# Optimization experiments

Hardware: AMD Instinct MI355X
Metric: run time of the kernel (lower is better)

## Reference

```python
import jax, jax.numpy as jnp
import numpy as np

N, D, H, C = 4096, 4096, 256, 16
NNZ_ATTR, E, NNZ_JM, NNZ_JA = 262144, 131072, 400000, 80000


def setup_inputs() -> dict:
    key = jax.random.key(0)
    ks = jax.random.split(key, 8)
    return {
        "attr_row": jax.random.randint(ks[0], (NNZ_ATTR,), 0, N),
        "attr_col": jax.random.randint(ks[1], (NNZ_ATTR,), 0, D),
        "edge_idx": jax.random.randint(ks[2], (2, E), 0, N),
        "j_mask_idx": jax.random.randint(ks[3], (2, NNZ_JM), 0, N),
        "jaug_mask_idx": jax.random.randint(ks[4], (2, NNZ_JA), 0, N),
        "lin1_w": jax.random.normal(ks[5], (H, D), dtype=jnp.float32) * (1.0 / np.sqrt(D)),
        "lin2_w": jax.random.normal(ks[6], (C, H), dtype=jnp.float32) * (1.0 / np.sqrt(H)),
        "bias2": jax.random.normal(ks[7], (C,), dtype=jnp.float32) * 0.01,
        "n": N,
        "d": D,
    }


def _gcn_norm_dense(a, n):
    # add remaining self loops (binary adjacency -> set diagonal to 1)
    idx = jnp.arange(n)
    a = a.at[idx, idx].set(1.0)
    # PyG gcn_norm: deg = scatter_add(weight, col) = column sums
    deg = a.sum(axis=0)
    dinv = jnp.where(deg > 0, jax.lax.rsqrt(deg), 0.0)
    # out[i] = sum_j dinv[i]*dinv[j]*A[j,i]*x[j]  ->  An = Dinv @ A^T @ Dinv
    return (dinv[:, None] * a.T) * dinv[None, :]


def reference(attr_row, attr_col, edge_idx, j_mask_idx, jaug_mask_idx,
              lin1_w, lin2_w, bias2, n, d):
    # --- edge augmentation: (edges AND J_mask) OR JAug_mask ---
    a = jnp.zeros((n, n), jnp.float32).at[edge_idx[0], edge_idx[1]].set(1.0)
    jm = jnp.zeros((n, n), bool).at[j_mask_idx[0], j_mask_idx[1]].set(True)
    ja = jnp.zeros((n, n), bool).at[jaug_mask_idx[0], jaug_mask_idx[1]].set(True)
    a_aug = jnp.maximum(jnp.where(jm, a, 0.0), ja.astype(jnp.float32))

    # --- layer 1: spmm(sparse binary X, W1^T), gcn_norm, propagate (no bias) ---
    x = jnp.zeros((n, d), jnp.float32).at[attr_row, attr_col].add(1.0)
    h = x @ lin1_w.T                     # [n, H]
    an = _gcn_norm_dense(a_aug, n)       # [n, n] normalized adjacency
    h = jax.nn.relu(an @ h)              # propagate + relu
    # dropout is identity in eval mode

    # --- layer 2: standard GCNConv with bias ---
    h2 = h @ lin2_w.T                    # [n, C]
    out = an @ h2 + bias2
    return out
```

## Files before the change

kernel.cpp:

```cpp
#include <hip/hip_runtime.h>

#define N_      4096
#define D_      4096
#define H_      256
#define C_      16
#define NNZ_ATTR 262144
#define E_      131072
#define NNZ_JM  400000
#define NNZ_JA  80000
#define WORDS   128
#define ADJ_STRIDE 128
#define ASTR    128
#define NT      256

typedef _Float16 half8v __attribute__((ext_vector_type(8)));
typedef _Float16 half2v __attribute__((ext_vector_type(2)));

#define OFF_EBT  ((size_t)0)
#define OFF_ABT  ((size_t)(2u<<20))
#define OFF_CNT  ((size_t)(4u<<20))
#define OFF_DINV (OFF_CNT + (size_t)(256u<<10))
#define OFF_DEG  (OFF_DINV + (size_t)(16u<<10))
#define OFF_CCOL (OFF_DEG + (size_t)(16u<<10))
#define OFF_ADJ  (OFF_CCOL + (size_t)(2u<<20))
#define OFF_W1T  (OFF_ADJ + (size_t)(2u<<20))
#define OFF_H1   (OFF_W1T + (size_t)(2u<<20))
#define OFF_H2   (OFF_H1  + (size_t)(2u<<20))

#define ZERO_BYTES ((size_t)((4u<<20)+(256u<<10)))
#define ZB_BLOCKS  1088
#define TR_BLOCKS  1024

#define SB_EDGE  1024
#define SB_JA    1536
#define SB_DIAG  1849
#define SB_TOTAL 1865

__global__ void k_pre(const float* __restrict__ w1, _Float16* __restrict__ w1t,
                      uint4* __restrict__ zp) {
    __shared__ float tile[32][33];
    int b = blockIdx.x, t = threadIdx.x;
    if (b < ZB_BLOCKS) {
        zp[(size_t)b * NT + t] = make_uint4(0u, 0u, 0u, 0u);
    } else {
        int bb = b - ZB_BLOCKS;
        int gx = bb & 127, gy = bb >> 7;
        int tx = t & 31, ty = t >> 5;
        int col = gx * 32 + tx;
        #pragma unroll
        for (int j = 0; j < 4; ++j)
            tile[ty + j * 8][tx] = w1[(size_t)(gy * 32 + ty + j * 8) * D_ + col];
        __syncthreads();
        int ocol = gy * 32 + tx;
        #pragma unroll
        for (int j = 0; j < 4; ++j)
            w1t[(size_t)(gx * 32 + ty + j * 8) * H_ + ocol] = (_Float16)tile[tx][ty + j * 8];
    }
}

__global__ void k_scat1(const int* __restrict__ attr_row, const int* __restrict__ attr_col,
                        const int* __restrict__ edge, const int* __restrict__ jaug,
                        unsigned* __restrict__ ebt, unsigned* __restrict__ abt,
                        unsigned* __restrict__ cnt, unsigned* __restrict__ ccol) {
    const int b = blockIdx.x, t = threadIdx.x;
    if (b < SB_EDGE) {
        int i = b * NT + t;
        int r = attr_row[i];
        unsigned pos = atomicAdd(&cnt[r << 4], 1u);
        if (pos < ASTR) ccol[(size_t)r * ASTR + pos] = (unsigned)attr_col[i];
    } else if (b < SB_JA) {
        int j = (b - SB_EDGE) * NT + t;
        int p = edge[j], q = edge[E_ + j];
        atomicOr(&ebt[(size_t)q * WORDS + (p >> 5)], 1u << (p & 31));
    } else if (b < SB_DIAG) {
        int j = (b - SB_JA) * NT + t;
        if (j < NNZ_JA) {
            int p = jaug[j], q = jaug[NNZ_JA + j];
            atomicOr(&abt[(size_t)q * WORDS + (p >> 5)], 1u << (p & 31));
        }
    } else {
        int r = (b - SB_DIAG) * NT + t;
        atomicOr(&abt[(size_t)r * WORDS + (r >> 5)], 1u << (r & 31));
    }
}

__global__ void k_scat2(const int* __restrict__ jmsk,
                        const unsigned* __restrict__ ebt, unsigned* __restrict__ abt) {
    int i = blockIdx.x * NT + threadIdx.x;
    if (i >= NNZ_JM) return;
    int p = jmsk[i], q = jmsk[NNZ_JM + i];
    size_t w = (size_t)q * WORDS + (p >> 5);
    if ((ebt[w] >> (p & 31)) & 1u)
        atomicOr(&abt[w], 1u << (p & 31));
}

__global__ void k_rowh1(const unsigned* __restrict__ abt, const unsigned* __restrict__ cnt,
                        const unsigned* __restrict__ ccol, const _Float16* __restrict__ w1t,
                        float* __restrict__ dinv, int* __restrict__ deg,
                        int* __restrict__ adj, _Float16* __restrict__ h1s) {
    __shared__ unsigned cols[128];
    __shared__ float part[4][2][32][8];
    __shared__ float sdinv[4];
    const int b = blockIdx.x, t = threadIdx.x;
    int wv = t >> 6, lane = t & 63;
    int q = 4 * b + wv;
    {
        uint2 m2 = ((const uint2*)(abt + (size_t)q * WORDS))[lane];
        unsigned w0 = m2.x, w1b = m2.y;
        int c = __popc(w0) + __popc(w1b);
        int pre = c;
        #pragma unroll
        for (int d2 = 1; d2 < 64; d2 <<= 1) {
            int x = __shfl_up(pre, d2);
            if (lane >= d2) pre += x;
        }
        int excl = pre - c;
        int total = __shfl(pre, 63);
        if (lane == 0) {
            float dv = rsqrtf((float)total);
            dinv[q] = dv;
            sdinv[wv] = dv;
            deg[q] = total < ADJ_STRIDE ? total : ADJ_STRIDE;
        }
        unsigned idx = (unsigned)excl;
        int* arow = adj + (size_t)q * ADJ_STRIDE;
        int base0 = lane * 64;
        while (w0)  { int bp = __ffs(w0) - 1;  w0  &= w0 - 1;  if (idx < ADJ_STRIDE) arow[idx] = base0 + bp;      ++idx; }
        while (w1b) { int bp = __ffs(w1b) - 1; w1b &= w1b - 1; if (idx < ADJ_STRIDE) arow[idx] = base0 + 32 + bp; ++idx; }
    }
    __syncthreads();
    int g = t >> 6, hw = (t >> 5) & 1, l32 = t & 31;
    for (int i = 0; i < 4; ++i) {
        int r = 4 * b + i;
        int m = (int)min(cnt[r << 4], (unsigned)ASTR);
        if (t < m) cols[t] = ccol[(size_t)r * ASTR + t];
        __syncthreads();
        float acc[8];
        #pragma unroll
        for (int e = 0; e < 8; ++e) acc[e] = 0.f;
        int sub = (g << 1) + hw;
        for (int j = 0; j < m; j += 8) {
            int jc = j + sub;
            if (jc < m) {
                unsigned c = cols[jc];
                half8v v = *(const half8v*)(w1t + (size_t)c * H_ + l32 * 8);
                #pragma unroll
                for (int e = 0; e < 8; ++e) acc[e] += (float)v[e];
            }
        }
        #pragma unroll
        for (int e = 0; e < 8; ++e) part[g][hw][l32][e] = acc[e];
        __syncthreads();
        int l = t >> 3, e = t & 7;
        float s = 0.f;
        #pragma unroll
        for (int gg = 0; gg < 4; ++gg) {
            s += part[gg][0][l][e];
            s += part[gg][1][l][e];
        }
        h1s[(size_t)r * H_ + t] = (_Float16)(s * sdinv[i]);
        __syncthreads();
    }
}

__global__ void k_prop1(const int* __restrict__ adj, const int* __restrict__ deg,
                        const float* __restrict__ dinv, const _Float16* __restrict__ h1s,
                        const float* __restrict__ w2, float* __restrict__ h2s) {
    __shared__ int adj_s[128];
    __shared__ float partial2[2][256];
    __shared__ float hrow[256];
    __shared__ float partial[16][17];
    const int b = blockIdx.x, t = threadIdx.x;
    int g2 = t >> 7, tt = t & 127;
    int c = t & 15, gg = t >> 4;
    float w2r[16];
    #pragma unroll
    for (int kk = 0; kk < 16; ++kk) w2r[kk] = w2[(size_t)c * H_ + gg * 16 + kk];
    for (int i = 0; i < 4; ++i) {
        int q = 4 * b + i;
        __syncthreads();
        if (t < ADJ_STRIDE) adj_s[t] = adj[(size_t)q * ADJ_STRIDE + t];
        __syncthreads();
        int dg = deg[q];
        float ax = 0.f, ay = 0.f;
        int j = g2;
        for (; j + 2 < dg; j += 4) {
            int p0 = adj_s[j], p1 = adj_s[j + 2];
            half2v v0 = *(const half2v*)(h1s + (size_t)p0 * H_ + tt * 2);
            half2v v1 = *(const half2v*)(h1s + (size_t)p1 * H_ + tt * 2);
            ax += (float)v0[0] + (float)v1[0];
            ay += (float)v0[1] + (float)v1[1];
        }
        for (; j < dg; j += 2) {
            int p0 = adj_s[j];
            half2v v0 = *(const half2v*)(h1s + (size_t)p0 * H_ + tt * 2);
            ax += (float)v0[0];
            ay += (float)v0[1];
        }
        partial2[g2][2 * tt]     = ax;
        partial2[g2][2 * tt + 1] = ay;
        __syncthreads();
        float dq = dinv[q];
        hrow[t] = fmaxf((partial2[0][t] + partial2[1][t]) * dq, 0.f);
        __syncthreads();
        float p = 0.f;
        #pragma unroll
        for (int kk = 0; kk < 16; ++kk) p += hrow[gg * 16 + kk] * w2r[kk];
        partial[gg][c] = p;
        __syncthreads();
        if (t < 16) {
            float s = 0.f;
            #pragma unroll
            for (int g3 = 0; g3 < 16; ++g3) s += partial[g3][t];
            h2s[(size_t)q * C_ + t] = s * dq;
        }
    }
}

__global__ void k_prop2(const int* __restrict__ adj, const int* __restrict__ deg,
                        const float* __restrict__ dinv, const float* __restrict__ h2s,
                        const float* __restrict__ bias, float* __restrict__ out) {
    const int b = blockIdx.x, t = threadIdx.x;
    int wv = t >> 6, lane = t & 63;
    int q = 4 * b + wv;
    int c = lane & 15, prt = lane >> 4;
    int dg = deg[q];
    const int* arow = adj + (size_t)q * ADJ_STRIDE;
    float acc = 0.f;
    for (int j = prt; j < dg; j += 4)
        acc += h2s[(size_t)arow[j] * C_ + c];
    acc += __shfl_down(acc, 32);
    acc += __shfl_down(acc, 16);
    if (lane < 16)
        out[(size_t)q * C_ + c] = dinv[q] * acc + bias[c];
}


extern "C" void kernel_launch(void* const* d_in, const int* in_sizes, int n_in,
                              void* d_out, int out_size, void* d_ws, size_t ws_size,
                              hipStream_t stream) {
    const int*   attr_row = (const int*)d_in[0];
    const int*   attr_col = (const int*)d_in[1];
    const int*   edge     = (const int*)d_in[2];
    const int*   jmsk     = (const int*)d_in[3];
    const int*   jaug     = (const int*)d_in[4];
    const float* w1       = (const float*)d_in[5];
    const float* w2       = (const float*)d_in[6];
    const float* bias2    = (const float*)d_in[7];
    float*       out      = (float*)d_out;

    char* ws = (char*)d_ws;
    unsigned*  ebt  = (unsigned*)(ws + OFF_EBT);
    unsigned*  abt  = (unsigned*)(ws + OFF_ABT);
    unsigned*  cnt  = (unsigned*)(ws + OFF_CNT);
    float*     dinv = (float*)(ws + OFF_DINV);
    int*       deg  = (int*)(ws + OFF_DEG);
    unsigned*  ccol = (unsigned*)(ws + OFF_CCOL);
    int*       adj  = (int*)(ws + OFF_ADJ);
    _Float16*  w1t  = (_Float16*)(ws + OFF_W1T);
    _Float16*  h1s  = (_Float16*)(ws + OFF_H1);
    float*     h2s  = (float*)(ws + OFF_H2);

    k_pre<<<ZB_BLOCKS + TR_BLOCKS, NT, 0, stream>>>(w1, w1t, (uint4*)d_ws);
    k_scat1<<<SB_TOTAL, NT, 0, stream>>>(attr_row, attr_col, edge, jaug,
                                         ebt, abt, cnt, ccol);
    k_scat2<<<(NNZ_JM + NT - 1) / NT, NT, 0, stream>>>(jmsk, ebt, abt);
    k_rowh1<<<N_ / 4, NT, 0, stream>>>(abt, cnt, ccol, w1t, dinv, deg, adj, h1s);
    k_prop1<<<N_ / 4, NT, 0, stream>>>(adj, deg, dinv, h1s, w2, h2s);
    k_prop2<<<N_ / 4, NT, 0, stream>>>(adj, deg, dinv, h2s, bias2, out);
}
```

Before: 75.46 us.

## Replace atomic bitmask scatters with dense byte maps and slot-claim dedup

After: 80.56 us. 6.8% more time.

```diff
diff --git a/kernel.cpp b/kernel.cpp
--- a/kernel.cpp
+++ b/kernel.cpp
@@ -10,40 +10,47 @@
 #define NNZ_JA  80000
 #define WORDS   128
 #define ADJ_STRIDE 128
-#define ASTR    128
 #define NT      256
+#define MAXCOLS 208
 
 typedef _Float16 half8v __attribute__((ext_vector_type(8)));
 typedef _Float16 half2v __attribute__((ext_vector_type(2)));
 
-#define OFF_EBT  ((size_t)0)
-#define OFF_ABT  ((size_t)(2u<<20))
-#define OFF_CNT  ((size_t)(4u<<20))
-#define OFF_DINV (OFF_CNT + (size_t)(256u<<10))
-#define OFF_DEG  (OFF_DINV + (size_t)(16u<<10))
-#define OFF_CCOL (OFF_DEG + (size_t)(16u<<10))
-#define OFF_ADJ  (OFF_CCOL + (size_t)(2u<<20))
-#define OFF_W1T  (OFF_ADJ + (size_t)(2u<<20))
-#define OFF_H1   (OFF_W1T + (size_t)(2u<<20))
-#define OFF_H2   (OFF_H1  + (size_t)(2u<<20))
-
-#define ZERO_BYTES ((size_t)((4u<<20)+(256u<<10)))
-#define ZB_BLOCKS  1088
+#define OFF_XSLOT ((size_t)0)
+#define OFF_EBB  ((size_t)64<<20)
+#define OFF_XB   (OFF_EBB + ((size_t)16<<20))
+#define OFF_ABT  (OFF_XB + ((size_t)16<<20))
+#define OFF_CNT  (OFF_ABT + ((size_t)2<<20))
+#define OFF_CCOL (OFF_CNT + ((size_t)16<<10))
+#define OFF_ADJ  (OFF_CCOL + ((size_t)256<<10))
+#define OFF_DINV (OFF_ADJ + ((size_t)2<<20))
+#define OFF_DEG  (OFF_DINV + ((size_t)16<<10))
+#define OFF_W1T  (OFF_DEG + ((size_t)16<<10))
+#define OFF_H1   (OFF_W1T + ((size_t)2<<20))
+#define OFF_H2   (OFF_H1 + ((size_t)2<<20))
+
+#define ZB_BLOCKS  8708
+#define XS_BLOCKS  1024
 #define TR_BLOCKS  1024
 
-#define SB_EDGE  1024
-#define SB_JA    1536
-#define SB_DIAG  1849
-#define SB_TOTAL 1865
+#define SC_ATTR  1024
+#define SC_EDGE  1536
+#define SC_JA    1849
+#define SC_TOT   1865
 
 __global__ void k_pre(const float* __restrict__ w1, _Float16* __restrict__ w1t,
-                      uint4* __restrict__ zp) {
+                      const int* __restrict__ attr_row, const int* __restrict__ attr_col,
+                      unsigned* __restrict__ xslot, uint4* __restrict__ zbase) {
     __shared__ float tile[32][33];
     int b = blockIdx.x, t = threadIdx.x;
     if (b < ZB_BLOCKS) {
-        zp[(size_t)b * NT + t] = make_uint4(0u, 0u, 0u, 0u);
+        zbase[(size_t)b * NT + t] = make_uint4(0u, 0u, 0u, 0u);
+    } else if (b < ZB_BLOCKS + XS_BLOCKS) {
+        int i = (b - ZB_BLOCKS) * NT + t;
+        int r = attr_row[i], c = attr_col[i];
+        xslot[(size_t)r * D_ + c] = (unsigned)i;
     } else {
-        int bb = b - ZB_BLOCKS;
+        int bb = b - ZB_BLOCKS - XS_BLOCKS;
         int gx = bb & 127, gy = bb >> 7;
         int tx = t & 31, ty = t >> 5;
         int col = gx * 32 + tx;
@@ -58,49 +65,56 @@
     }
 }
 
-__global__ void k_scat1(const int* __restrict__ attr_row, const int* __restrict__ attr_col,
-                        const int* __restrict__ edge, const int* __restrict__ jaug,
-                        unsigned* __restrict__ ebt, unsigned* __restrict__ abt,
-                        unsigned* __restrict__ cnt, unsigned* __restrict__ ccol) {
+__global__ void k_scat(const int* __restrict__ attr_row, const int* __restrict__ attr_col,
+                       const int* __restrict__ edge, const int* __restrict__ jaug,
+                       const unsigned* __restrict__ xslot,
+                       unsigned char* __restrict__ ebb, unsigned char* __restrict__ xb,
+                       unsigned* __restrict__ abt, unsigned* __restrict__ cnt,
+                       unsigned* __restrict__ ccol) {
     const int b = blockIdx.x, t = threadIdx.x;
-    if (b < SB_EDGE) {
+    if (b < SC_ATTR) {
         int i = b * NT + t;
-        int r = attr_row[i];
-        unsigned pos = atomicAdd(&cnt[r << 4], 1u);
-        if (pos < ASTR) ccol[(size_t)r * ASTR + pos] = (unsigned)attr_col[i];
-    } else if (b < SB_JA) {
-        int j = (b - SB_EDGE) * NT + t;
+        int r = attr_row[i], c = attr_col[i];
+        if (xslot[(size_t)r * D_ + c] == (unsigned)i) {
+            xb[(size_t)r * D_ + c] = 1;
+        } else {
+            unsigned pos = atomicAdd(&cnt[r], 1u);
+            if (pos < 16u) ccol[r * 16 + pos] = (unsigned)c;
+        }
+    } else if (b < SC_EDGE) {
+        int j = (b - SC_ATTR) * NT + t;
         int p = edge[j], q = edge[E_ + j];
-        atomicOr(&ebt[(size_t)q * WORDS + (p >> 5)], 1u << (p & 31));
-    } else if (b < SB_DIAG) {
-        int j = (b - SB_JA) * NT + t;
+        ebb[(size_t)q * N_ + p] = 1;
+    } else if (b < SC_JA) {
+        int j = (b - SC_EDGE) * NT + t;
         if (j < NNZ_JA) {
             int p = jaug[j], q = jaug[NNZ_JA + j];
             atomicOr(&abt[(size_t)q * WORDS + (p >> 5)], 1u << (p & 31));
         }
     } else {
-        int r = (b - SB_DIAG) * NT + t;
+        int r = (b - SC_JA) * NT + t;
         atomicOr(&abt[(size_t)r * WORDS + (r >> 5)], 1u << (r & 31));
     }
 }
 
-__global__ void k_scat2(const int* __restrict__ jmsk,
-                        const unsigned* __restrict__ ebt, unsigned* __restrict__ abt) {
+__global__ void k_probe(const int* __restrict__ jmsk,
+                        const unsigned char* __restrict__ ebb, unsigned* __restrict__ abt) {
     int i = blockIdx.x * NT + threadIdx.x;
     if (i >= NNZ_JM) return;
     int p = jmsk[i], q = jmsk[NNZ_JM + i];
-    size_t w = (size_t)q * WORDS + (p >> 5);
-    if ((ebt[w] >> (p & 31)) & 1u)
-        atomicOr(&abt[w], 1u << (p & 31));
-}
-
-__global__ void k_rowh1(const unsigned* __restrict__ abt, const unsigned* __restrict__ cnt,
-                        const unsigned* __restrict__ ccol, const _Float16* __restrict__ w1t,
+    if (ebb[(size_t)q * N_ + p])
+        atomicOr(&abt[(size_t)q * WORDS + (p >> 5)], 1u << (p & 31));
+}
+
+__global__ void k_rowh1(const unsigned* __restrict__ abt, const unsigned char* __restrict__ xb,
+                        const unsigned* __restrict__ cnt, const unsigned* __restrict__ ccol,
+                        const _Float16* __restrict__ w1t,
                         float* __restrict__ dinv, int* __restrict__ deg,
                         int* __restrict__ adj, _Float16* __restrict__ h1s) {
-    __shared__ unsigned cols[128];
+    __shared__ unsigned cols[MAXCOLS];
+    __shared__ int lcnt;
     __shared__ float part[4][2][32][8];
-    __shared__ float sdinv[4];
+    __shared__ float sdinv4[4];
     const int b = blockIdx.x, t = threadIdx.x;
     int wv = t >> 6, lane = t & 63;
     int q = 4 * b + wv;
@@ -119,7 +133,7 @@
         if (lane == 0) {
             float dv = rsqrtf((float)total);
             dinv[q] = dv;
-            sdinv[wv] = dv;
+            sdinv4[wv] = dv;
             deg[q] = total < ADJ_STRIDE ? total : ADJ_STRIDE;
         }
         unsigned idx = (unsigned)excl;
@@ -132,9 +146,30 @@
     int g = t >> 6, hw = (t >> 5) & 1, l32 = t & 31;
     for (int i = 0; i < 4; ++i) {
         int r = 4 * b + i;
-        int m = (int)min(cnt[r << 4], (unsigned)ASTR);
-        if (t < m) cols[t] = ccol[(size_t)r * ASTR + t];
-        __syncthreads();
+        if (t == 0) lcnt = 0;
+        __syncthreads();
+        uint4 xv = *(const uint4*)(xb + (size_t)r * D_ + t * 16);
+        unsigned wz[4] = {xv.x, xv.y, xv.z, xv.w};
+        #pragma unroll
+        for (int w4 = 0; w4 < 4; ++w4) {
+            unsigned u = wz[w4];
+            if (u) {
+                #pragma unroll
+                for (int bb = 0; bb < 4; ++bb) {
+                    if ((u >> (8 * bb)) & 0xffu) {
+                        int idx = atomicAdd(&lcnt, 1);
+                        if (idx < MAXCOLS) cols[idx] = t * 16 + w4 * 4 + bb;
+                    }
+                }
+            }
+        }
+        unsigned dn = cnt[r]; if (dn > 16u) dn = 16u;
+        if ((unsigned)t < dn) {
+            int idx = atomicAdd(&lcnt, 1);
+            if (idx < MAXCOLS) cols[idx] = ccol[r * 16 + t];
+        }
+        __syncthreads();
+        int m = lcnt < MAXCOLS ? lcnt : MAXCOLS;
         float acc[8];
         #pragma unroll
         for (int e = 0; e < 8; ++e) acc[e] = 0.f;
@@ -158,7 +193,7 @@
             s += part[gg][0][l][e];
             s += part[gg][1][l][e];
         }
-        h1s[(size_t)r * H_ + t] = (_Float16)(s * sdinv[i]);
+        h1s[(size_t)r * H_ + t] = (_Float16)(s * sdinv4[i]);
         __syncthreads();
     }
 }
@@ -250,22 +285,25 @@
     float*       out      = (float*)d_out;
 
     char* ws = (char*)d_ws;
-    unsigned*  ebt  = (unsigned*)(ws + OFF_EBT);
-    unsigned*  abt  = (unsigned*)(ws + OFF_ABT);
-    unsigned*  cnt  = (unsigned*)(ws + OFF_CNT);
-    float*     dinv = (float*)(ws + OFF_DINV);
-    int*       deg  = (int*)(ws + OFF_DEG);
-    unsigned*  ccol = (unsigned*)(ws + OFF_CCOL);
-    int*       adj  = (int*)(ws + OFF_ADJ);
-    _Float16*  w1t  = (_Float16*)(ws + OFF_W1T);
-    _Float16*  h1s  = (_Float16*)(ws + OFF_H1);
-    float*     h2s  = (float*)(ws + OFF_H2);
-
-    k_pre<<<ZB_BLOCKS + TR_BLOCKS, NT, 0, stream>>>(w1, w1t, (uint4*)d_ws);
-    k_scat1<<<SB_TOTAL, NT, 0, stream>>>(attr_row, attr_col, edge, jaug,
-                                         ebt, abt, cnt, ccol);
-    k_scat2<<<(NNZ_JM + NT - 1) / NT, NT, 0, stream>>>(jmsk, ebt, abt);
-    k_rowh1<<<N_ / 4, NT, 0, stream>>>(abt, cnt, ccol, w1t, dinv, deg, adj, h1s);
+    unsigned*      xslot = (unsigned*)(ws + OFF_XSLOT);
+    unsigned char* ebb   = (unsigned char*)(ws + OFF_EBB);
+    unsigned char* xb    = (unsigned char*)(ws + OFF_XB);
+    unsigned*      abt   = (unsigned*)(ws + OFF_ABT);
+    unsigned*      cnt   = (unsigned*)(ws + OFF_CNT);
+    unsigned*      ccol  = (unsigned*)(ws + OFF_CCOL);
+    int*           adj   = (int*)(ws + OFF_ADJ);
+    float*         dinv  = (float*)(ws + OFF_DINV);
+    int*           deg   = (int*)(ws + OFF_DEG);
+    _Float16*      w1t   = (_Float16*)(ws + OFF_W1T);
+    _Float16*      h1s   = (_Float16*)(ws + OFF_H1);
+    float*         h2s   = (float*)(ws + OFF_H2);
+
+    k_pre<<<ZB_BLOCKS + XS_BLOCKS + TR_BLOCKS, NT, 0, stream>>>(
+        w1, w1t, attr_row, attr_col, xslot, (uint4*)(ws + OFF_EBB));
+    k_scat<<<SC_TOT, NT, 0, stream>>>(attr_row, attr_col, edge, jaug, xslot,
+                                      ebb, xb, abt, cnt, ccol);
+    k_probe<<<(NNZ_JM + NT - 1) / NT, NT, 0, stream>>>(jmsk, ebb, abt);
+    k_rowh1<<<N_ / 4, NT, 0, stream>>>(abt, xb, cnt, ccol, w1t, dinv, deg, adj, h1s);
     k_prop1<<<N_ / 4, NT, 0, stream>>>(adj, deg, dinv, h1s, w2, h2s);
     k_prop2<<<N_ / 4, NT, 0, stream>>>(adj, deg, dinv, h2s, bias2, out);
 }
```

## Store attribute rows as bitmasks with duplicate list instead of atomic column lists

Applied to the files above, without the earlier changes.

Measured after the change: 77.50 us. +2.7%, slower.

```diff
diff --git a/kernel.cpp b/kernel.cpp
--- a/kernel.cpp
+++ b/kernel.cpp
@@ -10,38 +10,38 @@
 #define NNZ_JA  80000
 #define WORDS   128
 #define ADJ_STRIDE 128
-#define ASTR    128
 #define NT      256
+#define MAXCOLS 160
+#define DUPS    16
 
 typedef _Float16 half8v __attribute__((ext_vector_type(8)));
 typedef _Float16 half2v __attribute__((ext_vector_type(2)));
 
-#define OFF_EBT  ((size_t)0)
-#define OFF_ABT  ((size_t)(2u<<20))
-#define OFF_CNT  ((size_t)(4u<<20))
-#define OFF_DINV (OFF_CNT + (size_t)(256u<<10))
+#define OFF_XBIT ((size_t)0)
+#define OFF_EBT  ((size_t)(2u<<20))
+#define OFF_ABT  ((size_t)(4u<<20))
+#define OFF_DUPC ((size_t)(6u<<20))
+#define OFF_DUPL (OFF_DUPC + (size_t)(16u<<10))
+#define OFF_ADJ  (OFF_DUPL + (size_t)(256u<<10))
+#define OFF_DINV (OFF_ADJ + (size_t)(2u<<20))
 #define OFF_DEG  (OFF_DINV + (size_t)(16u<<10))
-#define OFF_CCOL (OFF_DEG + (size_t)(16u<<10))
-#define OFF_ADJ  (OFF_CCOL + (size_t)(2u<<20))
-#define OFF_W1T  (OFF_ADJ + (size_t)(2u<<20))
+#define OFF_W1T  (OFF_DEG + (size_t)(16u<<10))
 #define OFF_H1   (OFF_W1T + (size_t)(2u<<20))
-#define OFF_H2   (OFF_H1  + (size_t)(2u<<20))
-
-#define ZERO_BYTES ((size_t)((4u<<20)+(256u<<10)))
-#define ZB_BLOCKS  1088
+#define OFF_H2   (OFF_H1 + (size_t)(2u<<20))
+
+#define ZB_BLOCKS  1540
 #define TR_BLOCKS  1024
 
-#define SB_EDGE  1024
-#define SB_JA    1536
-#define SB_DIAG  1849
-#define SB_TOTAL 1865
+#define SC_ATTR  1024
+#define SC_EDGE  1536
+#define SC_TOT   1849
 
 __global__ void k_pre(const float* __restrict__ w1, _Float16* __restrict__ w1t,
-                      uint4* __restrict__ zp) {
+                      uint4* __restrict__ zbase) {
     __shared__ float tile[32][33];
     int b = blockIdx.x, t = threadIdx.x;
     if (b < ZB_BLOCKS) {
-        zp[(size_t)b * NT + t] = make_uint4(0u, 0u, 0u, 0u);
+        zbase[(size_t)b * NT + t] = make_uint4(0u, 0u, 0u, 0u);
     } else {
         int bb = b - ZB_BLOCKS;
         int gx = bb & 127, gy = bb >> 7;
@@ -58,33 +58,35 @@
     }
 }
 
-__global__ void k_scat1(const int* __restrict__ attr_row, const int* __restrict__ attr_col,
-                        const int* __restrict__ edge, const int* __restrict__ jaug,
-                        unsigned* __restrict__ ebt, unsigned* __restrict__ abt,
-                        unsigned* __restrict__ cnt, unsigned* __restrict__ ccol) {
-    const int b = blockIdx.x, t = threadIdx.x;
-    if (b < SB_EDGE) {
+__global__ void k_scat(const int* __restrict__ attr_row, const int* __restrict__ attr_col,
+                       const int* __restrict__ edge, const int* __restrict__ jaug,
+                       unsigned* __restrict__ xbit, unsigned* __restrict__ ebt,
+                       unsigned* __restrict__ abt, unsigned* __restrict__ dupc,
+                       unsigned* __restrict__ dupl) {
+    const int b = blockIdx.x, t = threadIdx.x;
+    if (b < SC_ATTR) {
         int i = b * NT + t;
-        int r = attr_row[i];
-        unsigned pos = atomicAdd(&cnt[r << 4], 1u);
-        if (pos < ASTR) ccol[(size_t)r * ASTR + pos] = (unsigned)attr_col[i];
-    } else if (b < SB_JA) {
-        int j = (b - SB_EDGE) * NT + t;
+        int r = attr_row[i], c = attr_col[i];
+        unsigned bit = 1u << (c & 31);
+        unsigned old = atomicOr(&xbit[(size_t)r * WORDS + (c >> 5)], bit);
+        if (old & bit) {
+            unsigned pos = atomicAdd(&dupc[r], 1u);
+            if (pos < DUPS) dupl[r * DUPS + pos] = (unsigned)c;
+        }
+    } else if (b < SC_EDGE) {
+        int j = (b - SC_ATTR) * NT + t;
         int p = edge[j], q = edge[E_ + j];
         atomicOr(&ebt[(size_t)q * WORDS + (p >> 5)], 1u << (p & 31));
-    } else if (b < SB_DIAG) {
-        int j = (b - SB_JA) * NT + t;
+    } else {
+        int j = (b - SC_EDGE) * NT + t;
         if (j < NNZ_JA) {
             int p = jaug[j], q = jaug[NNZ_JA + j];
             atomicOr(&abt[(size_t)q * WORDS + (p >> 5)], 1u << (p & 31));
         }
-    } else {
-        int r = (b - SB_DIAG) * NT + t;
-        atomicOr(&abt[(size_t)r * WORDS + (r >> 5)], 1u << (r & 31));
-    }
-}
-
-__global__ void k_scat2(const int* __restrict__ jmsk,
+    }
+}
+
+__global__ void k_probe(const int* __restrict__ jmsk,
                         const unsigned* __restrict__ ebt, unsigned* __restrict__ abt) {
     int i = blockIdx.x * NT + threadIdx.x;
     if (i >= NNZ_JM) return;
@@ -94,19 +96,25 @@
         atomicOr(&abt[w], 1u << (p & 31));
 }
 
-__global__ void k_rowh1(const unsigned* __restrict__ abt, const unsigned* __restrict__ cnt,
-                        const unsigned* __restrict__ ccol, const _Float16* __restrict__ w1t,
+__global__ void k_rowh1(const unsigned* __restrict__ abt, const unsigned* __restrict__ xbit,
+                        const unsigned* __restrict__ dupc, const unsigned* __restrict__ dupl,
+                        const _Float16* __restrict__ w1t,
                         float* __restrict__ dinv, int* __restrict__ deg,
                         int* __restrict__ adj, _Float16* __restrict__ h1s) {
-    __shared__ unsigned cols[128];
+    __shared__ unsigned cols[MAXCOLS];
+    __shared__ int lcnt;
     __shared__ float part[4][2][32][8];
-    __shared__ float sdinv[4];
+    __shared__ float sdinv4[4];
     const int b = blockIdx.x, t = threadIdx.x;
     int wv = t >> 6, lane = t & 63;
     int q = 4 * b + wv;
     {
         uint2 m2 = ((const uint2*)(abt + (size_t)q * WORDS))[lane];
         unsigned w0 = m2.x, w1b = m2.y;
+        int dw = q >> 5;
+        if ((dw >> 1) == lane) {
+            if (dw & 1) w1b |= 1u << (q & 31); else w0 |= 1u << (q & 31);
+        }
         int c = __popc(w0) + __popc(w1b);
         int pre = c;
         #pragma unroll
@@ -119,7 +127,7 @@
         if (lane == 0) {
             float dv = rsqrtf((float)total);
             dinv[q] = dv;
-            sdinv[wv] = dv;
+            sdinv4[wv] = dv;
             deg[q] = total < ADJ_STRIDE ? total : ADJ_STRIDE;
         }
         unsigned idx = (unsigned)excl;
@@ -132,9 +140,23 @@
     int g = t >> 6, hw = (t >> 5) & 1, l32 = t & 31;
     for (int i = 0; i < 4; ++i) {
         int r = 4 * b + i;
-        int m = (int)min(cnt[r << 4], (unsigned)ASTR);
-        if (t < m) cols[t] = ccol[(size_t)r * ASTR + t];
-        __syncthreads();
+        if (t == 0) lcnt = 0;
+        __syncthreads();
+        if (t < WORDS) {
+            unsigned u = xbit[(size_t)r * WORDS + t];
+            while (u) {
+                int bp = __ffs(u) - 1; u &= u - 1;
+                int idx = atomicAdd(&lcnt, 1);
+                if (idx < MAXCOLS) cols[idx] = (unsigned)(t * 32 + bp);
+            }
+        }
+        unsigned dn = dupc[r]; if (dn > (unsigned)DUPS) dn = DUPS;
+        if ((unsigned)t < dn) {
+            int idx = atomicAdd(&lcnt, 1);
+            if (idx < MAXCOLS) cols[idx] = dupl[r * DUPS + t];
+        }
+        __syncthreads();
+        int m = lcnt < MAXCOLS ? lcnt : MAXCOLS;
         float acc[8];
         #pragma unroll
         for (int e = 0; e < 8; ++e) acc[e] = 0.f;
@@ -158,7 +180,7 @@
             s += part[gg][0][l][e];
             s += part[gg][1][l][e];
         }
-        h1s[(size_t)r * H_ + t] = (_Float16)(s * sdinv[i]);
+        h1s[(size_t)r * H_ + t] = (_Float16)(s * sdinv4[i]);
         __syncthreads();
     }
 }
@@ -250,22 +272,23 @@
     float*       out      = (float*)d_out;
 
     char* ws = (char*)d_ws;
+    unsigned*  xbit = (unsigned*)(ws + OFF_XBIT);
     unsigned*  ebt  = (unsigned*)(ws + OFF_EBT);
     unsigned*  abt  = (unsigned*)(ws + OFF_ABT);
-    unsigned*  cnt  = (unsigned*)(ws + OFF_CNT);
+    unsigned*  dupc = (unsigned*)(ws + OFF_DUPC);
+    unsigned*  dupl = (unsigned*)(ws + OFF_DUPL);
+    int*       adj  = (int*)(ws + OFF_ADJ);
     float*     dinv = (float*)(ws + OFF_DINV);
     int*       deg  = (int*)(ws + OFF_DEG);
-    unsigned*  ccol = (unsigned*)(ws + OFF_CCOL);
-    int*       adj  = (int*)(ws + OFF_ADJ);
     _Float16*  w1t  = (_Float16*)(ws + OFF_W1T);
     _Float16*  h1s  = (_Float16*)(ws + OFF_H1);
     float*     h2s  = (float*)(ws + OFF_H2);
 
     k_pre<<<ZB_BLOCKS + TR_BLOCKS, NT, 0, stream>>>(w1, w1t, (uint4*)d_ws);
-    k_scat1<<<SB_TOTAL, NT, 0, stream>>>(attr_row, attr_col, edge, jaug,
-                                         ebt, abt, cnt, ccol);
-    k_scat2<<<(NNZ_JM + NT - 1) / NT, NT, 0, stream>>>(jmsk, ebt, abt);
-    k_rowh1<<<N_ / 4, NT, 0, stream>>>(abt, cnt, ccol, w1t, dinv, deg, adj, h1s);
+    k_scat<<<SC_TOT, NT, 0, stream>>>(attr_row, attr_col, edge, jaug,
+                                      xbit, ebt, abt, dupc, dupl);
+    k_probe<<<(NNZ_JM + NT - 1) / NT, NT, 0, stream>>>(jmsk, ebt, abt);
+    k_rowh1<<<N_ / 4, NT, 0, stream>>>(abt, xbit, dupc, dupl, w1t, dinv, deg, adj, h1s);
     k_prop1<<<N_ / 4, NT, 0, stream>>>(adj, deg, dinv, h1s, w2, h2s);
     k_prop2<<<N_ / 4, NT, 0, stream>>>(adj, deg, dinv, h2s, bias2, out);
 }
```
